# Kernel optimization log

Hardware: AMD Instinct MI355X
Metric: run time of the kernel (lower is better)

Reference implementation:

```python
import jax, jax.numpy as jnp
import numpy as np

HIDDEN = 1024
VOCAB = 32000
NUM_EXPERTS = 8
RANK = 4
ALPHA = 1.0
TOP_K = 2
TEMP = 1.0
KV_CACHE_SIZE = 2048
CACHE_DEC = 128
CACHE_SIZES = [KV_CACHE_SIZE - CACHE_DEC * i for i in range(NUM_EXPERTS)]  # pyramidal allocation
B, S = 2, 1024


def setup_inputs() -> dict:
    key = jax.random.key(0)
    ks = jax.random.split(key, 16)
    sd = 0.02
    return {
        'x': jax.random.randint(ks[0], (B, S), 0, VOCAB),
        'embedding': jax.random.normal(ks[1], (VOCAB, HIDDEN), jnp.float32) * sd,
        'gate_w': jax.random.normal(ks[2], (HIDDEN, NUM_EXPERTS), jnp.float32) * sd,
        'gate_b': jnp.zeros((NUM_EXPERTS,), jnp.float32),
        'expert_w': jax.random.normal(ks[3], (NUM_EXPERTS, HIDDEN, HIDDEN), jnp.float32) * sd,
        'expert_b': jnp.zeros((NUM_EXPERTS, HIDDEN), jnp.float32),
        'expert_la': jax.random.normal(ks[4], (NUM_EXPERTS, HIDDEN, RANK), jnp.float32) * sd,
        'expert_lb': jax.random.normal(ks[5], (NUM_EXPERTS, RANK, HIDDEN), jnp.float32) * sd,
        'cache_values': jax.random.normal(ks[6], (NUM_EXPERTS, KV_CACHE_SIZE, HIDDEN), jnp.float32),
        'cache_importance': jax.random.uniform(ks[7], (NUM_EXPERTS, KV_CACHE_SIZE), jnp.float32),
        'cache_la': jax.random.normal(ks[8], (NUM_EXPERTS, HIDDEN, RANK), jnp.float32) * sd,
        'cache_lb': jax.random.normal(ks[9], (NUM_EXPERTS, RANK, HIDDEN), jnp.float32) * sd,
        'vocab_w': jax.random.normal(ks[10], (HIDDEN, VOCAB), jnp.float32) * sd,
        'vocab_b': jnp.zeros((VOCAB,), jnp.float32),
    }


def _cache_get_all(cache_values, cache_importance, cache_la, cache_lb):
    """Pyramid compressor: keep top-50% slots by importance, apply value LoRA, mean-pool -> [E, H]."""
    scale = ALPHA / RANK
    vecs = []
    for e in range(NUM_EXPERTS):
        n = CACHE_SIZES[e]
        k = n // 2  # compression_ratio = 0.5
        _, idx = jax.lax.top_k(cache_importance[e, :n], k)
        cv = cache_values[e, :n][idx]                      # [k, H] irregular gather
        cv = cv + (cv @ cache_la[e]) @ cache_lb[e] * scale  # value LoRA
        vecs.append(cv.mean(axis=0))
    return jnp.stack(vecs)  # [E, H]


def reference(x, embedding, gate_w, gate_b, expert_w, expert_b, expert_la, expert_lb,
              cache_values, cache_importance, cache_la, cache_lb, vocab_w, vocab_b):
    scale = ALPHA / RANK
    h = embedding[x]  # [B, S, H]
    # AdaptiveRouter: softmax gate, top-2, renormalize, scatter to dense weights
    gate_logits = (h @ gate_w + gate_b) / TEMP
    probs = jax.nn.softmax(gate_logits, axis=-1)            # [B, S, E]
    top_vals, top_idx = jax.lax.top_k(probs, TOP_K)
    top_w = top_vals / top_vals.sum(axis=-1, keepdims=True)
    routing_weights = (jax.nn.one_hot(top_idx, NUM_EXPERTS, dtype=h.dtype)
                       * top_w[..., None]).sum(axis=-2)     # [B, S, E]
    # LoRA experts: base linear + low-rank update, all experts at once
    exp_out = (jnp.einsum('bsh,ehf->bsef', h, expert_w) + expert_b
               + jnp.einsum('bsh,ehr,erf->bsef', h, expert_la, expert_lb) * scale)  # [B,S,E,H]
    # Per-expert pyramidal KV-cache contribution (broadcast vector)
    cache_vecs = _cache_get_all(cache_values, cache_importance, cache_la, cache_lb)  # [E, H]
    expert_output = jnp.einsum('bsef,bse->bsf', exp_out + cache_vecs[None, None], routing_weights)
    logits = expert_output @ vocab_w + vocab_b  # [B, S, V]
    return logits
```

## Files before the change

### kernel.cpp

```cpp
#include <hip/hip_runtime.h>

typedef unsigned short u16;
typedef __bf16 bf16x8 __attribute__((ext_vector_type(8)));
typedef float f32x4 __attribute__((ext_vector_type(4)));

#define HDIM 1024
#define VDIM 32000
#define NEXP 8
#define NTOK 2048
#define LSCALE 0.25f

__device__ __forceinline__ float bf2f(u16 v) {
  union { unsigned u; float f; } x; x.u = ((unsigned)v) << 16; return x.f;
}
__device__ __forceinline__ u16 f2bf(float f) {
  union { float f; unsigned u; } x; x.f = f;
  return (u16)((x.u + 0x7fffu + ((x.u >> 16) & 1u)) >> 16);
}
__device__ __forceinline__ float lde(const void* p, size_t i, int isf32) {
  if (isf32) return ((const float*)p)[i];
  else       return bf2f(((const u16*)p)[i]);
}

__device__ __forceinline__ void gload16(const u16* g, u16* l) {
  __builtin_amdgcn_global_load_lds(
      (const __attribute__((address_space(1))) void*)g,
      (__attribute__((address_space(3))) void*)l, 16, 0, 0);
}

__global__ __launch_bounds__(256) void detect_dtype(const u16* __restrict__ emb,
                                                    int* __restrict__ flag) {
  __shared__ int cnt;
  int tid = threadIdx.x;
  if (tid == 0) cnt = 0;
  __syncthreads();
  int sane = 0;
  for (int i = tid; i < 1024; i += 256) {
    u16 v = emb[2 * i];
    int ex = (v >> 7) & 0xff;
    sane += (ex >= 87 && ex <= 127) ? 1 : 0;
  }
  atomicAdd(&cnt, sane);
  __syncthreads();
  if (tid == 0) *flag = (cnt < 512) ? 1 : 0;
}

__global__ __launch_bounds__(256) void transpose_lora(
    const void* __restrict__ W, u16* __restrict__ WT,
    const void* __restrict__ la, const void* __restrict__ lb,
    int K, int N, int hasLora, int ncol0, const int* __restrict__ flag) {
  int isf32 = *flag;
  int tk = blockIdx.x * 64;
  int tn = ncol0 + blockIdx.y * 64;
  int e  = blockIdx.z;
  __shared__ alignas(16) u16 tile[64][72];
  int tid = threadIdx.x;
  int row = tid >> 2, c0l = (tid & 3) * 16;
  size_t src = (size_t)e * K * N + (size_t)(tk + row) * N + tn + c0l;
  u16 tmp[16];
  if (isf32) {
    const float* Wf = (const float*)W;
#pragma unroll
    for (int j = 0; j < 4; ++j) {
      float4 f = *(const float4*)(Wf + src + j * 4);
      tmp[j * 4 + 0] = f2bf(f.x); tmp[j * 4 + 1] = f2bf(f.y);
      tmp[j * 4 + 2] = f2bf(f.z); tmp[j * 4 + 3] = f2bf(f.w);
    }
  } else {
    const u16* Wh = (const u16*)W;
    *(uint4*)&tmp[0] = *(const uint4*)(Wh + src);
    *(uint4*)&tmp[8] = *(const uint4*)(Wh + src + 8);
  }
  *(uint4*)&tile[row][c0l] = *(uint4*)&tmp[0];
  *(uint4*)&tile[row][c0l + 8] = *(uint4*)&tmp[8];
  __syncthreads();
  int f = tid >> 2;
  int h0 = (tid & 3) * 16;
  float lbv[4];
  if (hasLora) {
#pragma unroll
    for (int r = 0; r < 4; ++r)
      lbv[r] = lde(lb, (size_t)e * 4 * N + (size_t)r * N + tn + f, isf32);
  }
  u16 outv[16];
#pragma unroll
  for (int i = 0; i < 16; ++i) {
    float x = bf2f(tile[h0 + i][f]);
    if (hasLora) {
      size_t lbase = ((size_t)e * K + tk + h0 + i) * 4;
      float s = 0.f;
#pragma unroll
      for (int r = 0; r < 4; ++r) s += lde(la, lbase + r, isf32) * lbv[r];
      x += LSCALE * s;
    }
    outv[i] = f2bf(x);
  }
  u16* dst = WT + (size_t)e * K * N + (size_t)(blockIdx.y * 64 + f) * K + tk + h0;
  *(uint4*)dst = *(uint4*)&outv[0];
  *(uint4*)(dst + 8) = *(uint4*)&outv[8];
}

__global__ __launch_bounds__(256) void embed_gate(
    const int* __restrict__ x, const void* __restrict__ emb,
    const void* __restrict__ gw, const void* __restrict__ gb,
    u16* __restrict__ h_bf, int* __restrict__ tope, float* __restrict__ topw,
    const int* __restrict__ flag) {
  int isf32 = *flag;
  int t = blockIdx.x, tid = threadIdx.x;
  __shared__ float hs[HDIM];
  __shared__ float gl[NEXP];
  int idx = x[t];
  if (isf32) {
    const float* er = (const float*)emb + (size_t)idx * HDIM;
    float4 f = ((const float4*)er)[tid];
    u16 h4[4] = { f2bf(f.x), f2bf(f.y), f2bf(f.z), f2bf(f.w) };
    ((uint2*)(h_bf + (size_t)t * HDIM))[tid] = *(uint2*)h4;
    hs[tid * 4 + 0] = f.x; hs[tid * 4 + 1] = f.y;
    hs[tid * 4 + 2] = f.z; hs[tid * 4 + 3] = f.w;
  } else {
    uint2 v = ((const uint2*)((const u16*)emb + (size_t)idx * HDIM))[tid];
    ((uint2*)(h_bf + (size_t)t * HDIM))[tid] = v;
    hs[tid * 4 + 0] = bf2f((u16)(v.x & 0xffffu));
    hs[tid * 4 + 1] = bf2f((u16)(v.x >> 16));
    hs[tid * 4 + 2] = bf2f((u16)(v.y & 0xffffu));
    hs[tid * 4 + 3] = bf2f((u16)(v.y >> 16));
  }
  __syncthreads();
  int wid = tid >> 6, lane = tid & 63;
  int c0 = wid * 2, c1 = c0 + 1;
  float p0 = 0.f, p1 = 0.f;
  for (int i = lane; i < HDIM; i += 64) {
    float hv = hs[i];
    p0 += hv * lde(gw, (size_t)i * 8 + c0, isf32);
    p1 += hv * lde(gw, (size_t)i * 8 + c1, isf32);
  }
#pragma unroll
  for (int off = 32; off; off >>= 1) {
    p0 += __shfl_down(p0, off, 64);
    p1 += __shfl_down(p1, off, 64);
  }
  if (lane == 0) { gl[c0] = p0 + lde(gb, c0, isf32); gl[c1] = p1 + lde(gb, c1, isf32); }
  __syncthreads();
  if (tid == 0) {
    float mx = gl[0];
#pragma unroll
    for (int e = 1; e < NEXP; ++e) mx = fmaxf(mx, gl[e]);
    float pe[NEXP];
#pragma unroll
    for (int e = 0; e < NEXP; ++e) pe[e] = expf(gl[e] - mx);
    int i1 = 0;
#pragma unroll
    for (int e = 1; e < NEXP; ++e) if (pe[e] > pe[i1]) i1 = e;
    int i2 = (i1 == 0) ? 1 : 0;
#pragma unroll
    for (int e = 0; e < NEXP; ++e) if (e != i1 && pe[e] > pe[i2]) i2 = e;
    float s2 = pe[i1] + pe[i2];
    tope[t] = i1 | (i2 << 8);
    topw[t * 2 + 0] = pe[i1] / s2;
    topw[t * 2 + 1] = pe[i2] / s2;
  }
}

__global__ __launch_bounds__(256) void cache_select(
    const void* __restrict__ imp, short* __restrict__ listg,
    const int* __restrict__ flag) {
  int isf32 = *flag;
  int e = blockIdx.x, tid = threadIdx.x;
  int n = 2048 - 128 * e, k = n >> 1;
  __shared__ unsigned keys[2048];
  __shared__ int hist[256];
  __shared__ short list[1024];
  __shared__ unsigned s_prefix;
  __shared__ int s_above;
  __shared__ int cnt_gt, cnt_tie;
  for (int i = tid; i < n; i += 256) {
    if (isf32) {
      union { float f; unsigned u; } c; c.f = ((const float*)imp)[e * 2048 + i];
      keys[i] = c.u;
    } else {
      keys[i] = ((unsigned)((const u16*)imp)[e * 2048 + i]) << 16;
    }
  }
  if (tid == 0) { cnt_gt = 0; cnt_tie = 0; }
  __syncthreads();
  unsigned prefix = 0; int above = 0;
  for (int level = 3; level >= 0; --level) {
    hist[tid] = 0;
    __syncthreads();
    for (int i = tid; i < n; i += 256) {
      unsigned kk = keys[i];
      bool m = (level == 3) || ((kk >> ((level + 1) * 8)) == prefix);
      if (m) atomicAdd(&hist[(kk >> (level * 8)) & 255], 1);
    }
    __syncthreads();
    if (tid == 0) {
      int cum = 0, b = 255;
      for (; b > 0; --b) { int h = hist[b]; if (above + cum + h >= k) break; cum += h; }
      s_above = above + cum;
      s_prefix = (prefix << 8) | (unsigned)b;
    }
    __syncthreads();
    prefix = s_prefix; above = s_above;
  }
  int need = k - above;
  for (int i = tid; i < n; i += 256) {
    if (keys[i] > prefix) { int p = atomicAdd(&cnt_gt, 1); list[p] = (short)i; }
  }
  __syncthreads();
  for (int i = tid; i < n; i += 256) {
    if (keys[i] == prefix) {
      int r = 0;
      for (int j = 0; j < i; ++j) r += (keys[j] == prefix) ? 1 : 0;
      if (r < need) { int p = atomicAdd(&cnt_tie, 1); list[above + p] = (short)i; }
    }
  }
  __syncthreads();
  for (int i = tid; i < k; i += 256) listg[e * 1024 + i] = list[i];
}

__global__ __launch_bounds__(256) void cache_pool(
    const void* __restrict__ cv, const short* __restrict__ listg,
    float* __restrict__ mean, const int* __restrict__ flag) {
  int isf32 = *flag;
  int e = blockIdx.x, s = blockIdx.y, tid = threadIdx.x;
  int n = 2048 - 128 * e, k = n >> 1;
  int rg = tid >> 4, ct = tid & 15;
  int f0 = s * 64 + ct * 4;
  __shared__ short lists[1024];
  __shared__ float red[16][64];
  for (int i = tid; i < k; i += 256) lists[i] = listg[e * 1024 + i];
  __syncthreads();
  float a0 = 0.f, a1 = 0.f, a2 = 0.f, a3 = 0.f;
  if (isf32) {
    const float* cvf = (const float*)cv;
    for (int j = rg; j < k; j += 16) {
      int row = lists[j];
      float4 vv = *(const float4*)(cvf + ((size_t)e * 2048 + row) * HDIM + f0);
      a0 += vv.x; a1 += vv.y; a2 += vv.z; a3 += vv.w;
    }
  } else {
    const u16* cvh = (const u16*)cv;
    for (int j = rg; j < k; j += 16) {
      int row = lists[j];
      uint2 vv = *(const uint2*)(cvh + ((size_t)e * 2048 + row) * HDIM + f0);
      a0 += bf2f((u16)(vv.x & 0xffffu));
      a1 += bf2f((u16)(vv.x >> 16));
      a2 += bf2f((u16)(vv.y & 0xffffu));
      a3 += bf2f((u16)(vv.y >> 16));
    }
  }
  red[rg][ct * 4 + 0] = a0;
  red[rg][ct * 4 + 1] = a1;
  red[rg][ct * 4 + 2] = a2;
  red[rg][ct * 4 + 3] = a3;
  __syncthreads();
  if (tid < 64) {
    float sm = 0.f;
#pragma unroll
    for (int r = 0; r < 16; ++r) sm += red[r][tid];
    mean[(size_t)e * HDIM + s * 64 + tid] = sm / (float)k;
  }
}

__global__ __launch_bounds__(256) void cache_finalize(
    const float* __restrict__ mean, const void* __restrict__ cla,
    const void* __restrict__ clb, const void* __restrict__ eb,
    float* __restrict__ ec, const int* __restrict__ flag) {
  int isf32 = *flag;
  int e = blockIdx.x, tid = threadIdx.x;
  __shared__ float tmp4[4];
  if (tid < 4) tmp4[tid] = 0.f;
  __syncthreads();
  int f0 = tid * 4;
  float m[4];
#pragma unroll
  for (int i = 0; i < 4; ++i) m[i] = mean[(size_t)e * HDIM + f0 + i];
#pragma unroll
  for (int r = 0; r < 4; ++r) {
    float pr = 0.f;
#pragma unroll
    for (int i = 0; i < 4; ++i)
      pr += m[i] * lde(cla, ((size_t)e * HDIM + f0 + i) * 4 + r, isf32);
    atomicAdd(&tmp4[r], pr);
  }
  __syncthreads();
#pragma unroll
  for (int i = 0; i < 4; ++i) {
    int f = f0 + i;
    float add = 0.f;
#pragma unroll
    for (int r = 0; r < 4; ++r)
      add += tmp4[r] * lde(clb, (size_t)e * 4 * HDIM + r * HDIM + f, isf32);
    ec[e * HDIM + f] = m[i] + LSCALE * add + lde(eb, (size_t)e * HDIM + f, isf32);
  }
}

__global__ __launch_bounds__(256) void route_build(
    const int* __restrict__ tope, u16* __restrict__ elist, int* __restrict__ ecnt) {
  int e = blockIdx.x;
  __shared__ int c;
  if (threadIdx.x == 0) c = 0;
  __syncthreads();
  for (int t = threadIdx.x; t < NTOK; t += 256) {
    int pe = tope[t];
    int e1 = pe & 255, e2 = (pe >> 8) & 255;
    if (e1 == e) { int p = atomicAdd(&c, 1); elist[e * NTOK + p] = (u16)t; }
    else if (e2 == e) { int p = atomicAdd(&c, 1); elist[e * NTOK + p] = (u16)(t | 0x8000); }
  }
  __syncthreads();
  if (threadIdx.x == 0) ecnt[e] = c;
}

__global__ __launch_bounds__(256) void gemm_expert_gather(
    const u16* __restrict__ A, const u16* __restrict__ Bt,
    const float* __restrict__ topw, const u16* __restrict__ elist,
    const int* __restrict__ ecnt, const float* __restrict__ ec,
    float* __restrict__ slot0, float* __restrict__ slot1) {
  const int K = HDIM;
  int mc = blockIdx.x, n0 = blockIdx.y * 128, e = blockIdx.z;
  int cnt = ecnt[e];
  int r0 = mc * 64;
  if (r0 >= cnt) return;
  __shared__ alignas(16) u16 As[64 * 32];
  __shared__ alignas(16) u16 Bs[128 * 32];
  int tid = threadIdx.x, lane = tid & 63, wid = tid >> 6;
  int wm = wid >> 1, wn = wid & 1;
  int q = lane >> 4, lr = lane & 15;
  int srow = wid * 16 + (lane >> 2);
  int scol = (lane & 3) * 8;
  int li = r0 + srow; if (li >= cnt) li = r0;
  int tokme = elist[e * NTOK + li] & 2047;
  const u16* Ag = A + (size_t)tokme * K + scol;
  const u16* Bg = Bt + (size_t)e * K * HDIM + (size_t)(n0 + srow) * K + scol;
  u16* AsL = As + wid * 16 * 32;
  u16* BsL = Bs + wid * 16 * 32;
  f32x4 acc[2][4];
#pragma unroll
  for (int mi = 0; mi < 2; ++mi)
#pragma unroll
    for (int ni = 0; ni < 4; ++ni) acc[mi][ni] = (f32x4){0.f, 0.f, 0.f, 0.f};
  for (int kt = 0; kt < K / 32; ++kt) {
    __syncthreads();
    gload16(Ag + kt * 32, AsL);
    gload16(Bg + kt * 32, BsL);
    gload16(Bg + (size_t)64 * K + kt * 32, BsL + 64 * 32);
    __syncthreads();
    bf16x8 af[2], bfr[4];
#pragma unroll
    for (int mi = 0; mi < 2; ++mi)
      af[mi] = *(const bf16x8*)(As + (wm * 32 + mi * 16 + lr) * 32 + q * 8);
#pragma unroll
    for (int ni = 0; ni < 4; ++ni)
      bfr[ni] = *(const bf16x8*)(Bs + (wn * 64 + ni * 16 + lr) * 32 + q * 8);
#pragma unroll
    for (int mi = 0; mi < 2; ++mi)
#pragma unroll
      for (int ni = 0; ni < 4; ++ni)
        acc[mi][ni] = __builtin_amdgcn_mfma_f32_16x16x32_bf16(af[mi], bfr[ni], acc[mi][ni], 0, 0, 0);
  }
#pragma unroll
  for (int mi = 0; mi < 2; ++mi) {
#pragma unroll
    for (int r = 0; r < 4; ++r) {
      int lrow = wm * 32 + mi * 16 + q * 4 + r;
      int gi = r0 + lrow;
      if (gi >= cnt) continue;
      int ent = elist[e * NTOK + gi];
      int t2 = ent & 2047, sl = ent >> 15;
      float w = topw[t2 * 2 + sl];
      float* dst = sl ? slot1 : slot0;
#pragma unroll
      for (int ni = 0; ni < 4; ++ni) {
        int col = n0 + wn * 64 + ni * 16 + lr;
        dst[(size_t)t2 * HDIM + col] = w * (acc[mi][ni][r] + ec[e * HDIM + col]);
      }
    }
  }
}

__global__ __launch_bounds__(256) void combine_outh(
    const float* __restrict__ s0, const float* __restrict__ s1,
    u16* __restrict__ outh) {
  int i = blockIdx.x * 256 + threadIdx.x;
  float4 a = ((const float4*)s0)[i];
  float4 b = ((const float4*)s1)[i];
  u16 o[4] = { f2bf(a.x + b.x), f2bf(a.y + b.y), f2bf(a.z + b.z), f2bf(a.w + b.w) };
  ((uint2*)outh)[i] = *(uint2*)o;
}

__global__ __launch_bounds__(512) void gemm_vocab(
    const u16* __restrict__ A, const u16* __restrict__ Bt,
    const void* __restrict__ bias, void* __restrict__ outp,
    int n0base, const int* __restrict__ flag) {
  int isf32 = *flag;
  const int K = HDIM, N = VDIM;
  int nwg = gridDim.x;
  int per = nwg >> 3;
  int newid = (blockIdx.x & 7) * per + (blockIdx.x >> 3);
  int bn = newid >> 3, bm = newid & 7;
  int m0 = bm * 256, n0l = bn * 256;
  __shared__ alignas(16) u16 As[256 * 32];
  __shared__ alignas(16) u16 Bs[256 * 32];
  int tid = threadIdx.x, lane = tid & 63, wid = tid >> 6;
  int wm = wid >> 2, wn = wid & 3;
  int q = lane >> 4, lr = lane & 15;
  int prow = lane >> 2;
  int lgran = (lane & 3) ^ (prow & 3);
  int srow = wid * 16 + prow;
  const u16* Ag  = A  + (size_t)(m0 + srow) * K + lgran * 8;
  const u16* Ag2 = A  + (size_t)(m0 + 128 + srow) * K + lgran * 8;
  const u16* Bg  = Bt + (size_t)(n0l + srow) * K + lgran * 8;
  const u16* Bg2 = Bt + (size_t)(n0l + 128 + srow) * K + lgran * 8;
  u16* AsL = As + wid * 16 * 32;
  u16* BsL = Bs + wid * 16 * 32;
  f32x4 acc[8][4];
#pragma unroll
  for (int mi = 0; mi < 8; ++mi)
#pragma unroll
    for (int ni = 0; ni < 4; ++ni) acc[mi][ni] = (f32x4){0.f, 0.f, 0.f, 0.f};

  for (int kt = 0; kt < K / 32; ++kt) {
    __syncthreads();
    gload16(Ag  + kt * 32, AsL);
    gload16(Ag2 + kt * 32, AsL + 128 * 32);
    gload16(Bg  + kt * 32, BsL);
    gload16(Bg2 + kt * 32, BsL + 128 * 32);
    __syncthreads();
    bf16x8 af[8], bfr[4];
#pragma unroll
    for (int mi = 0; mi < 8; ++mi) {
      int row = wm * 128 + mi * 16 + lr;
      af[mi] = *(const bf16x8*)(As + row * 32 + ((q ^ (row & 3)) * 8));
    }
#pragma unroll
    for (int ni = 0; ni < 4; ++ni) {
      int row = wn * 64 + ni * 16 + lr;
      bfr[ni] = *(const bf16x8*)(Bs + row * 32 + ((q ^ (row & 3)) * 8));
    }
#pragma unroll
    for (int mi = 0; mi < 8; ++mi)
#pragma unroll
      for (int ni = 0; ni < 4; ++ni)
        acc[mi][ni] = __builtin_amdgcn_mfma_f32_16x16x32_bf16(af[mi], bfr[ni], acc[mi][ni], 0, 0, 0);
  }
#pragma unroll
  for (int ni = 0; ni < 4; ++ni) {
    int col = n0base + n0l + wn * 64 + ni * 16 + lr;
    float vb = lde(bias, col, isf32);
#pragma unroll
    for (int mi = 0; mi < 8; ++mi) {
#pragma unroll
      for (int r = 0; r < 4; ++r) {
        int row = m0 + wm * 128 + mi * 16 + q * 4 + r;
        float val = acc[mi][ni][r] + vb;
        if (isf32) ((float*)outp)[(size_t)row * N + col] = val;
        else       ((u16*)outp)[(size_t)row * N + col] = f2bf(val);
      }
    }
  }
}

extern "C" void kernel_launch(void* const* d_in, const int* in_sizes, int n_in,
                              void* d_out, int out_size, void* d_ws, size_t ws_size,
                              hipStream_t stream) {
  const int*  x    = (const int*)d_in[0];
  const void* emb  = d_in[1];
  const void* gw   = d_in[2];
  const void* gb   = d_in[3];
  const void* ew   = d_in[4];
  const void* eb   = d_in[5];
  const void* ela  = d_in[6];
  const void* elb  = d_in[7];
  const void* cv   = d_in[8];
  const void* imp  = d_in[9];
  const void* cla  = d_in[10];
  const void* clb  = d_in[11];
  const void* vw   = d_in[12];
  const void* vb   = d_in[13];

  char* ws = (char*)d_ws;
  u16*   WeffT = (u16*)(ws);
  u16*   h_bf  = (u16*)(ws + 16777216);
  u16*   outh  = (u16*)(ws + 20971520);
  float* ec    = (float*)(ws + 25165824);
  int*   flag  = (int*)(ws + 25198592);
  float* mean  = (float*)(ws + 25198656);
  short* listg = (short*)(ws + 25231424);
  int*   tope  = (int*)(ws + 25247808);
  float* topw  = (float*)(ws + 25256000);
  u16*   elist = (u16*)(ws + 25272384);
  int*   ecnt  = (int*)(ws + 25305152);
  float* slot0 = (float*)(ws + 25305216);
  float* slot1 = (float*)(ws + 33693824);
  u16*   chunk = (u16*)(ws + 42082432);

  long long avail = (long long)ws_size - 42082432LL;
  long long cc = (avail > 0) ? (avail / (HDIM * 2)) : 0;
  cc &= ~255LL;
  if (cc > 16384) cc = 16384;
  if (cc < 256) cc = 256;
  int chunkcols = (int)cc;

  detect_dtype<<<dim3(1), 256, 0, stream>>>((const u16*)emb, flag);
  transpose_lora<<<dim3(HDIM / 64, HDIM / 64, NEXP), 256, 0, stream>>>(
      ew, WeffT, ela, elb, HDIM, HDIM, 1, 0, flag);
  embed_gate<<<dim3(NTOK), 256, 0, stream>>>(x, emb, gw, gb, h_bf, tope, topw, flag);
  cache_select<<<dim3(NEXP), 256, 0, stream>>>(imp, listg, flag);
  cache_pool<<<dim3(NEXP, 16), 256, 0, stream>>>(cv, listg, mean, flag);
  cache_finalize<<<dim3(NEXP), 256, 0, stream>>>(mean, cla, clb, eb, ec, flag);
  route_build<<<dim3(NEXP), 256, 0, stream>>>(tope, elist, ecnt);
  gemm_expert_gather<<<dim3(32, 8, NEXP), 256, 0, stream>>>(
      h_bf, WeffT, topw, elist, ecnt, ec, slot0, slot1);
  combine_outh<<<dim3(NTOK * HDIM / 4 / 256), 256, 0, stream>>>(slot0, slot1, outh);
  for (int c0 = 0; c0 < VDIM; c0 += chunkcols) {
    int nc = (VDIM - c0 < chunkcols) ? (VDIM - c0) : chunkcols;
    transpose_lora<<<dim3(HDIM / 64, nc / 64, 1), 256, 0, stream>>>(
        vw, chunk, nullptr, nullptr, HDIM, VDIM, 0, c0, flag);
    gemm_vocab<<<dim3((nc / 256) * 8), 512, 0, stream>>>(
        outh, chunk, vb, d_out, c0, flag);
  }
}
```

Baseline: 921.7 us.

## Pipeline vocab GEMM with multi-stage LDS buffering, parallelize cache select and pool

The vocab GEMM drops its two-barrier single-stage loop for a 64-wide K tile with double-buffered LDS (128KB) and prefetches issued between MFMA phases, plus explicit vmcnt waits, barriers and setprio. The aim is to hide global-load latency behind MFMA work. Separately, the radix-select bucket search is parallelized across threads instead of run by thread 0, cache_pool runs twice as many blocks, and the chunk cap now allows a single vocab chunk. The large LDS footprint cuts occupancy to one block per CU, and the hand-placed waitcnt values must match the exact order of loads in flight.

```diff
diff --git a/kernel.cpp b/kernel.cpp
--- a/kernel.cpp
+++ b/kernel.cpp
@@ -26,6 +26,15 @@
   __builtin_amdgcn_global_load_lds(
       (const __attribute__((address_space(1))) void*)g,
       (__attribute__((address_space(3))) void*)l, 16, 0, 0);
+}
+
+#define SBAR() do { __builtin_amdgcn_s_barrier(); __builtin_amdgcn_sched_barrier(0); } while (0)
+#define WAITLGKM() do { asm volatile("s_waitcnt lgkmcnt(0)" ::: "memory"); __builtin_amdgcn_sched_barrier(0); } while (0)
+template<int N> __device__ __forceinline__ void waitvm() {
+  if constexpr (N == 6) asm volatile("s_waitcnt vmcnt(6)" ::: "memory");
+  else if constexpr (N == 2) asm volatile("s_waitcnt vmcnt(2)" ::: "memory");
+  else asm volatile("s_waitcnt vmcnt(0)" ::: "memory");
+  __builtin_amdgcn_sched_barrier(0);
 }
 
 __global__ __launch_bounds__(256) void detect_dtype(const u16* __restrict__ emb,
@@ -193,14 +202,19 @@
       if (m) atomicAdd(&hist[(kk >> (level * 8)) & 255], 1);
     }
     __syncthreads();
-    if (tid == 0) {
-      int cum = 0, b = 255;
-      for (; b > 0; --b) { int h = hist[b]; if (above + cum + h >= k) break; cum += h; }
-      s_above = above + cum;
-      s_prefix = (prefix << 8) | (unsigned)b;
+    {
+      int needl = k - above;
+      int S = 0;
+      for (int j = tid; j < 256; ++j) S += hist[j];
+      int Snext = S - hist[tid];
+      if (S >= needl && (tid == 255 || Snext < needl)) {
+        s_above = above + Snext;
+        s_prefix = (prefix << 8) | (unsigned)tid;
+      }
     }
     __syncthreads();
     prefix = s_prefix; above = s_above;
+    __syncthreads();
   }
   int need = k - above;
   for (int i = tid; i < n; i += 256) {
@@ -224,23 +238,23 @@
   int isf32 = *flag;
   int e = blockIdx.x, s = blockIdx.y, tid = threadIdx.x;
   int n = 2048 - 128 * e, k = n >> 1;
-  int rg = tid >> 4, ct = tid & 15;
-  int f0 = s * 64 + ct * 4;
+  int rg = tid >> 3, ct = tid & 7;
+  int f0 = s * 32 + ct * 4;
   __shared__ short lists[1024];
-  __shared__ float red[16][64];
+  __shared__ float red[32][32];
   for (int i = tid; i < k; i += 256) lists[i] = listg[e * 1024 + i];
   __syncthreads();
   float a0 = 0.f, a1 = 0.f, a2 = 0.f, a3 = 0.f;
   if (isf32) {
     const float* cvf = (const float*)cv;
-    for (int j = rg; j < k; j += 16) {
+    for (int j = rg; j < k; j += 32) {
       int row = lists[j];
       float4 vv = *(const float4*)(cvf + ((size_t)e * 2048 + row) * HDIM + f0);
       a0 += vv.x; a1 += vv.y; a2 += vv.z; a3 += vv.w;
     }
   } else {
     const u16* cvh = (const u16*)cv;
-    for (int j = rg; j < k; j += 16) {
+    for (int j = rg; j < k; j += 32) {
       int row = lists[j];
       uint2 vv = *(const uint2*)(cvh + ((size_t)e * 2048 + row) * HDIM + f0);
       a0 += bf2f((u16)(vv.x & 0xffffu));
@@ -254,11 +268,11 @@
   red[rg][ct * 4 + 2] = a2;
   red[rg][ct * 4 + 3] = a3;
   __syncthreads();
-  if (tid < 64) {
+  if (tid < 32) {
     float sm = 0.f;
 #pragma unroll
-    for (int r = 0; r < 16; ++r) sm += red[r][tid];
-    mean[(size_t)e * HDIM + s * 64 + tid] = sm / (float)k;
+    for (int r = 0; r < 32; ++r) sm += red[r][tid];
+    mean[(size_t)e * HDIM + s * 32 + tid] = sm / (float)k;
   }
 }
 
@@ -388,6 +402,91 @@
   ((uint2*)outh)[i] = *(uint2*)o;
 }
 
+#define VNT 16
+
+template<int VM2, int VM4, bool S12, bool S34>
+__device__ __forceinline__ void vtile(
+    int t, u16* lds, int wid,
+    const u16* pA0, const u16* pA1, const u16* pB0, const u16* pB1,
+    int aoff, int boff, f32x4 (&acc)[8][4]) {
+  int buf = t & 1, obuf = buf ^ 1;
+  const u16* As0 = lds + (buf * 2 + 0) * 8192;
+  const u16* As1 = lds + (buf * 2 + 1) * 8192;
+  const u16* Bs0 = lds + 32768 + (buf * 2 + 0) * 8192;
+  const u16* Bs1 = lds + 32768 + (buf * 2 + 1) * 8192;
+  bf16x8 af[4], bfr[4];
+#pragma unroll
+  for (int ni = 0; ni < 4; ++ni) bfr[ni] = *(const bf16x8*)(Bs0 + boff + ni * 512);
+#pragma unroll
+  for (int j = 0; j < 4; ++j) af[j] = *(const bf16x8*)(As0 + aoff + j * 512);
+  if (S12) {
+    u16* d = lds + (obuf * 2 + 1) * 8192 + wid * 512;
+    gload16(pA0 + (t + 1) * 64 + 32, d);
+    gload16(pA1 + (t + 1) * 64 + 32, d + 4096);
+  }
+  SBAR(); WAITLGKM();
+  __builtin_amdgcn_s_setprio(1);
+#pragma unroll
+  for (int j = 0; j < 4; ++j)
+#pragma unroll
+    for (int ni = 0; ni < 4; ++ni)
+      acc[j][ni] = __builtin_amdgcn_mfma_f32_16x16x32_bf16(af[j], bfr[ni], acc[j][ni], 0, 0, 0);
+  __builtin_amdgcn_s_setprio(0);
+  SBAR();
+#pragma unroll
+  for (int j = 0; j < 4; ++j) af[j] = *(const bf16x8*)(As0 + aoff + (4 + j) * 512);
+  if (S12) {
+    u16* d = lds + 32768 + (obuf * 2 + 1) * 8192 + wid * 512;
+    gload16(pB0 + (t + 1) * 64 + 32, d);
+    gload16(pB1 + (t + 1) * 64 + 32, d + 4096);
+  }
+  waitvm<VM2>();
+  SBAR(); WAITLGKM();
+  __builtin_amdgcn_s_setprio(1);
+#pragma unroll
+  for (int j = 0; j < 4; ++j)
+#pragma unroll
+    for (int ni = 0; ni < 4; ++ni)
+      acc[4 + j][ni] = __builtin_amdgcn_mfma_f32_16x16x32_bf16(af[j], bfr[ni], acc[4 + j][ni], 0, 0, 0);
+  __builtin_amdgcn_s_setprio(0);
+  SBAR();
+#pragma unroll
+  for (int ni = 0; ni < 4; ++ni) bfr[ni] = *(const bf16x8*)(Bs1 + boff + ni * 512);
+#pragma unroll
+  for (int j = 0; j < 4; ++j) af[j] = *(const bf16x8*)(As1 + aoff + j * 512);
+  if (S34) {
+    u16* d = lds + (buf * 2 + 0) * 8192 + wid * 512;
+    gload16(pA0 + (t + 2) * 64, d);
+    gload16(pA1 + (t + 2) * 64, d + 4096);
+  }
+  SBAR(); WAITLGKM();
+  __builtin_amdgcn_s_setprio(1);
+#pragma unroll
+  for (int j = 0; j < 4; ++j)
+#pragma unroll
+    for (int ni = 0; ni < 4; ++ni)
+      acc[j][ni] = __builtin_amdgcn_mfma_f32_16x16x32_bf16(af[j], bfr[ni], acc[j][ni], 0, 0, 0);
+  __builtin_amdgcn_s_setprio(0);
+  SBAR();
+#pragma unroll
+  for (int j = 0; j < 4; ++j) af[j] = *(const bf16x8*)(As1 + aoff + (4 + j) * 512);
+  if (S34) {
+    u16* d = lds + 32768 + (buf * 2 + 0) * 8192 + wid * 512;
+    gload16(pB0 + (t + 2) * 64, d);
+    gload16(pB1 + (t + 2) * 64, d + 4096);
+  }
+  waitvm<VM4>();
+  SBAR(); WAITLGKM();
+  __builtin_amdgcn_s_setprio(1);
+#pragma unroll
+  for (int j = 0; j < 4; ++j)
+#pragma unroll
+    for (int ni = 0; ni < 4; ++ni)
+      acc[4 + j][ni] = __builtin_amdgcn_mfma_f32_16x16x32_bf16(af[j], bfr[ni], acc[4 + j][ni], 0, 0, 0);
+  __builtin_amdgcn_s_setprio(0);
+  SBAR();
+}
+
 __global__ __launch_bounds__(512) void gemm_vocab(
     const u16* __restrict__ A, const u16* __restrict__ Bt,
     const void* __restrict__ bias, void* __restrict__ outp,
@@ -399,50 +498,46 @@
   int newid = (blockIdx.x & 7) * per + (blockIdx.x >> 3);
   int bn = newid >> 3, bm = newid & 7;
   int m0 = bm * 256, n0l = bn * 256;
-  __shared__ alignas(16) u16 As[256 * 32];
-  __shared__ alignas(16) u16 Bs[256 * 32];
+  __shared__ alignas(1024) u16 lds[65536];
   int tid = threadIdx.x, lane = tid & 63, wid = tid >> 6;
   int wm = wid >> 2, wn = wid & 3;
   int q = lane >> 4, lr = lane & 15;
-  int prow = lane >> 2;
-  int lgran = (lane & 3) ^ (prow & 3);
-  int srow = wid * 16 + prow;
-  const u16* Ag  = A  + (size_t)(m0 + srow) * K + lgran * 8;
-  const u16* Ag2 = A  + (size_t)(m0 + 128 + srow) * K + lgran * 8;
-  const u16* Bg  = Bt + (size_t)(n0l + srow) * K + lgran * 8;
-  const u16* Bg2 = Bt + (size_t)(n0l + 128 + srow) * K + lgran * 8;
-  u16* AsL = As + wid * 16 * 32;
-  u16* BsL = Bs + wid * 16 * 32;
+  int colsw = (q ^ ((lr >> 1) & 3)) * 8;
+  int aoff = wm * 4096 + lr * 32 + colsw;
+  int boff = wn * 2048 + lr * 32 + colsw;
+  int srl = lane >> 2;
+  int ssw = ((lane & 3) ^ ((srl >> 1) & 3)) * 8;
+  const u16* pA0 = A + (size_t)(m0 + wid * 16 + srl) * K + ssw;
+  const u16* pA1 = A + (size_t)(m0 + (8 + wid) * 16 + srl) * K + ssw;
+  const u16* pB0 = Bt + (size_t)(n0l + wid * 16 + srl) * K + ssw;
+  const u16* pB1 = Bt + (size_t)(n0l + (8 + wid) * 16 + srl) * K + ssw;
   f32x4 acc[8][4];
 #pragma unroll
   for (int mi = 0; mi < 8; ++mi)
 #pragma unroll
     for (int ni = 0; ni < 4; ++ni) acc[mi][ni] = (f32x4){0.f, 0.f, 0.f, 0.f};
-
-  for (int kt = 0; kt < K / 32; ++kt) {
-    __syncthreads();
-    gload16(Ag  + kt * 32, AsL);
-    gload16(Ag2 + kt * 32, AsL + 128 * 32);
-    gload16(Bg  + kt * 32, BsL);
-    gload16(Bg2 + kt * 32, BsL + 128 * 32);
-    __syncthreads();
-    bf16x8 af[8], bfr[4];
-#pragma unroll
-    for (int mi = 0; mi < 8; ++mi) {
-      int row = wm * 128 + mi * 16 + lr;
-      af[mi] = *(const bf16x8*)(As + row * 32 + ((q ^ (row & 3)) * 8));
-    }
-#pragma unroll
-    for (int ni = 0; ni < 4; ++ni) {
-      int row = wn * 64 + ni * 16 + lr;
-      bfr[ni] = *(const bf16x8*)(Bs + row * 32 + ((q ^ (row & 3)) * 8));
-    }
-#pragma unroll
-    for (int mi = 0; mi < 8; ++mi)
-#pragma unroll
-      for (int ni = 0; ni < 4; ++ni)
-        acc[mi][ni] = __builtin_amdgcn_mfma_f32_16x16x32_bf16(af[mi], bfr[ni], acc[mi][ni], 0, 0, 0);
-  }
+  {
+    u16* dA0 = lds + 0 * 8192 + wid * 512;
+    u16* dB0 = lds + 32768 + 0 * 8192 + wid * 512;
+    u16* dA1 = lds + 1 * 8192 + wid * 512;
+    u16* dB1 = lds + 32768 + 1 * 8192 + wid * 512;
+    u16* eA0 = lds + 2 * 8192 + wid * 512;
+    u16* eB0 = lds + 32768 + 2 * 8192 + wid * 512;
+    gload16(pA0 + 0, dA0);       gload16(pA1 + 0, dA0 + 4096);
+    gload16(pB0 + 0, dB0);       gload16(pB1 + 0, dB0 + 4096);
+    gload16(pA0 + 32, dA1);      gload16(pA1 + 32, dA1 + 4096);
+    gload16(pB0 + 32, dB1);      gload16(pB1 + 32, dB1 + 4096);
+    gload16(pA0 + 64, eA0);      gload16(pA1 + 64, eA0 + 4096);
+    gload16(pB0 + 64, eB0);      gload16(pB1 + 64, eB0 + 4096);
+    asm volatile("s_waitcnt vmcnt(4)" ::: "memory");
+    __builtin_amdgcn_sched_barrier(0);
+    SBAR();
+  }
+#pragma unroll 2
+  for (int t = 0; t < VNT - 2; ++t)
+    vtile<6, 6, true, true>(t, lds, wid, pA0, pA1, pB0, pB1, aoff, boff, acc);
+  vtile<6, 2, true, false>(VNT - 2, lds, wid, pA0, pA1, pB0, pB1, aoff, boff, acc);
+  vtile<0, 0, false, false>(VNT - 1, lds, wid, pA0, pA1, pB0, pB1, aoff, boff, acc);
 #pragma unroll
   for (int ni = 0; ni < 4; ++ni) {
     int col = n0base + n0l + wn * 64 + ni * 16 + lr;
@@ -497,7 +592,7 @@
   long long avail = (long long)ws_size - 42082432LL;
   long long cc = (avail > 0) ? (avail / (HDIM * 2)) : 0;
   cc &= ~255LL;
-  if (cc > 16384) cc = 16384;
+  if (cc > VDIM) cc = VDIM;
   if (cc < 256) cc = 256;
   int chunkcols = (int)cc;
 
@@ -506,7 +601,7 @@
       ew, WeffT, ela, elb, HDIM, HDIM, 1, 0, flag);
   embed_gate<<<dim3(NTOK), 256, 0, stream>>>(x, emb, gw, gb, h_bf, tope, topw, flag);
   cache_select<<<dim3(NEXP), 256, 0, stream>>>(imp, listg, flag);
-  cache_pool<<<dim3(NEXP, 16), 256, 0, stream>>>(cv, listg, mean, flag);
+  cache_pool<<<dim3(NEXP, 32), 256, 0, stream>>>(cv, listg, mean, flag);
   cache_finalize<<<dim3(NEXP), 256, 0, stream>>>(mean, cla, clb, eb, ec, flag);
   route_build<<<dim3(NEXP), 256, 0, stream>>>(tope, elist, ecnt);
   gemm_expert_gather<<<dim3(32, 8, NEXP), 256, 0, stream>>>(
```

Result: faster. 840.3 us (-8.8%).
